# Kernel tuning notes

Hardware: AMD Instinct MI355X
Metric: run time of the kernel (lower is better)

Reference implementation:

```python
import jax, jax.numpy as jnp
import numpy as np

N, K_, D_ = 16384, 32, 128

def setup_inputs() -> dict:
    key = jax.random.key(0)
    k1, k2, k3 = jax.random.split(key, 3)
    x = jax.random.normal(k1, (1, N, D_), dtype=jnp.float32)
    codes = jax.random.normal(k2, (K_, D_), dtype=jnp.float32)
    scale = jax.random.uniform(k3, (K_,), dtype=jnp.float32)
    return {"x": x, "codes": codes, "scale": scale}

def reference(x, codes, scale):
    # x: (1, N, D) -> residuals R: (N, K, D)
    R = x[0][:, None, :] - codes[None, :, :]
    # scaled L2 norm (NOT squared) over D, scaled per-codeword by `scale`
    l2 = jnp.linalg.norm(R, axis=-1)            # (N, K)
    W = jax.nn.softmax(l2 * scale, axis=-1)     # softmax over K
    # aggregated encoding: (K, D)
    E = jnp.einsum('nk,nkd->kd', W, R)
    return E
```

## Files before the change

kernel.cpp:

```cpp
#include <hip/hip_runtime.h>

constexpr int N    = 16384;
constexpr int K    = 32;
constexpr int D    = 128;
constexpr int SPAD = K + 2;

typedef float f4 __attribute__((ext_vector_type(4)));

template <int CTRL>
__device__ __forceinline__ float dpp_add(float v) {
    int j = __builtin_amdgcn_update_dpp(0, __float_as_int(v), CTRL, 0xF, 0xF, false);
    return v + __int_as_float(j);
}
__device__ __forceinline__ float sum16(float v) {
    v = dpp_add<0xB1>(v);
    v = dpp_add<0x4E>(v);
    v = dpp_add<0x141>(v);
    v = dpp_add<0x140>(v);
    return v;
}

__global__ __launch_bounds__(256) void enc_partial(
    const float* __restrict__ x,
    const float* __restrict__ codes,
    const float* __restrict__ scale,
    float* __restrict__ ws,
    int nchunk)
{
    __shared__ float sc_lds[8][SPAD];
    __shared__ float w_lds[8][SPAD];

    const int tid = threadIdx.x;
    const int kg  = tid >> 4;
    const int dg  = tid & 15;
    const int d4  = dg << 2;
    const int k0  = kg << 1;

    const float4 cA0 = *reinterpret_cast<const float4*>(&codes[k0 * D + d4]);
    const float4 cA1 = *reinterpret_cast<const float4*>(&codes[k0 * D + 64 + d4]);
    const float4 cB0 = *reinterpret_cast<const float4*>(&codes[(k0 + 1) * D + d4]);
    const float4 cB1 = *reinterpret_cast<const float4*>(&codes[(k0 + 1) * D + 64 + d4]);
    const float sA = scale[k0];
    const float sB = scale[k0 + 1];

    float4 tA0 = make_float4(0.f, 0.f, 0.f, 0.f);
    float4 tA1 = tA0, tB0 = tA0, tB1 = tA0;
    float swA = 0.f, swB = 0.f;

    const float* xb = x + (long)blockIdx.x * nchunk * 8 * D;

    for (int c = 0; c < nchunk; ++c) {
        float4 xr[8][2];
        const float* xc = xb + c * 8 * D;
        #pragma unroll
        for (int n = 0; n < 8; ++n) {
            xr[n][0] = *reinterpret_cast<const float4*>(xc + n * D + d4);
            xr[n][1] = *reinterpret_cast<const float4*>(xc + n * D + 64 + d4);
        }

        #pragma unroll
        for (int n = 0; n < 8; ++n) {
            const float4 xa = xr[n][0];
            const float4 xb4 = xr[n][1];
            float r;
            float pA0 = 0.f, pA1 = 0.f, pB0 = 0.f, pB1 = 0.f;
            r = xa.x - cA0.x;  pA0 = fmaf(r, r, pA0);
            r = xa.y - cA0.y;  pA1 = fmaf(r, r, pA1);
            r = xa.z - cA0.z;  pA0 = fmaf(r, r, pA0);
            r = xa.w - cA0.w;  pA1 = fmaf(r, r, pA1);
            r = xb4.x - cA1.x; pA0 = fmaf(r, r, pA0);
            r = xb4.y - cA1.y; pA1 = fmaf(r, r, pA1);
            r = xb4.z - cA1.z; pA0 = fmaf(r, r, pA0);
            r = xb4.w - cA1.w; pA1 = fmaf(r, r, pA1);
            r = xa.x - cB0.x;  pB0 = fmaf(r, r, pB0);
            r = xa.y - cB0.y;  pB1 = fmaf(r, r, pB1);
            r = xa.z - cB0.z;  pB0 = fmaf(r, r, pB0);
            r = xa.w - cB0.w;  pB1 = fmaf(r, r, pB1);
            r = xb4.x - cB1.x; pB0 = fmaf(r, r, pB0);
            r = xb4.y - cB1.y; pB1 = fmaf(r, r, pB1);
            r = xb4.z - cB1.z; pB0 = fmaf(r, r, pB0);
            r = xb4.w - cB1.w; pB1 = fmaf(r, r, pB1);
            float pA = sum16(pA0 + pA1);
            float pB = sum16(pB0 + pB1);
            if (dg == 0) {
                sc_lds[n][k0]     = sqrtf(pA) * sA;
                sc_lds[n][k0 + 1] = sqrtf(pB) * sB;
            }
        }
        __syncthreads();

        {
            const int row = tid >> 5;
            const int q   = tid & 31;
            float s = sc_lds[row][q];
            float m = s;
            m = fmaxf(m, __shfl_xor(m, 1));
            m = fmaxf(m, __shfl_xor(m, 2));
            m = fmaxf(m, __shfl_xor(m, 4));
            m = fmaxf(m, __shfl_xor(m, 8));
            m = fmaxf(m, __shfl_xor(m, 16));
            const float LOG2E = 1.44269504088896f;
            float e = exp2f((s - m) * LOG2E);
            float sum = e;
            sum += __shfl_xor(sum, 1);
            sum += __shfl_xor(sum, 2);
            sum += __shfl_xor(sum, 4);
            sum += __shfl_xor(sum, 8);
            sum += __shfl_xor(sum, 16);
            w_lds[row][q] = e * (1.0f / sum);
        }
        __syncthreads();

        #pragma unroll
        for (int n = 0; n < 8; ++n) {
            const float2 w = *reinterpret_cast<const float2*>(&w_lds[n][k0]);
            const float4 xa = xr[n][0];
            const float4 xb4 = xr[n][1];
            tA0.x = fmaf(w.x, xa.x, tA0.x);
            tA0.y = fmaf(w.x, xa.y, tA0.y);
            tA0.z = fmaf(w.x, xa.z, tA0.z);
            tA0.w = fmaf(w.x, xa.w, tA0.w);
            tA1.x = fmaf(w.x, xb4.x, tA1.x);
            tA1.y = fmaf(w.x, xb4.y, tA1.y);
            tA1.z = fmaf(w.x, xb4.z, tA1.z);
            tA1.w = fmaf(w.x, xb4.w, tA1.w);
            tB0.x = fmaf(w.y, xa.x, tB0.x);
            tB0.y = fmaf(w.y, xa.y, tB0.y);
            tB0.z = fmaf(w.y, xa.z, tB0.z);
            tB0.w = fmaf(w.y, xa.w, tB0.w);
            tB1.x = fmaf(w.y, xb4.x, tB1.x);
            tB1.y = fmaf(w.y, xb4.y, tB1.y);
            tB1.z = fmaf(w.y, xb4.z, tB1.z);
            tB1.w = fmaf(w.y, xb4.w, tB1.w);
            swA += w.x;
            swB += w.y;
        }
        __syncthreads();
    }

    f4* o = reinterpret_cast<f4*>(ws + (long)blockIdx.x * (K * D) + k0 * D + d4);
    f4 e0 = { tA0.x - swA * cA0.x, tA0.y - swA * cA0.y,
              tA0.z - swA * cA0.z, tA0.w - swA * cA0.w };
    f4 e1 = { tA1.x - swA * cA1.x, tA1.y - swA * cA1.y,
              tA1.z - swA * cA1.z, tA1.w - swA * cA1.w };
    f4 e2 = { tB0.x - swB * cB0.x, tB0.y - swB * cB0.y,
              tB0.z - swB * cB0.z, tB0.w - swB * cB0.w };
    f4 e3 = { tB1.x - swB * cB1.x, tB1.y - swB * cB1.y,
              tB1.z - swB * cB1.z, tB1.w - swB * cB1.w };
    __builtin_nontemporal_store(e0, o);
    __builtin_nontemporal_store(e1, o + 16);
    __builtin_nontemporal_store(e2, o + 32);
    __builtin_nontemporal_store(e3, o + 48);
}

__global__ __launch_bounds__(256) void reduce2(
    const float* __restrict__ ws, float* __restrict__ out, int nrows)
{
    __shared__ f4 part[64][4];

    const int tid   = threadIdx.x;
    const int col   = tid & 3;
    const int slice = tid >> 2;
    const int gcol  = blockIdx.x * 4 + col;
    const int rpt   = nrows >> 6;

    const f4* P = reinterpret_cast<const f4*>(ws);
    f4 acc = { 0.f, 0.f, 0.f, 0.f };
    long base = (long)slice * rpt * 1024 + gcol;
    for (int r = 0; r < rpt; ++r) {
        f4 v = __builtin_nontemporal_load(P + base + (long)r * 1024);
        acc += v;
    }
    part[slice][col] = acc;
    __syncthreads();

    #pragma unroll
    for (int stride = 32; stride >= 1; stride >>= 1) {
        if (tid < stride * 4) {
            part[slice][col] += part[slice + stride][col];
        }
        __syncthreads();
    }
    if (tid < 4) {
        reinterpret_cast<f4*>(out)[blockIdx.x * 4 + tid] = part[0][tid];
    }
}

extern "C" void kernel_launch(void* const* d_in, const int* in_sizes, int n_in,
                              void* d_out, int out_size, void* d_ws, size_t ws_size,
                              hipStream_t stream) {
    const float* x     = (const float*)d_in[0];
    const float* codes = (const float*)d_in[1];
    const float* scale = (const float*)d_in[2];
    float* out = (float*)d_out;
    float* ws  = (float*)d_ws;

    int grid1 = 512;
    if (ws_size < (size_t)grid1 * K * D * sizeof(float)) grid1 = 128;
    const int nchunk = N / (grid1 * 8);

    enc_partial<<<grid1, 256, 0, stream>>>(x, codes, scale, ws, nchunk);
    reduce2<<<256, 256, 0, stream>>>(ws, out, grid1);
}
```

Measured before the change: 29.26 us.

## Expand squared distance via dot products, double-buffer LDS, use DPP reductions, enlarge grid

Computes the squared distance as |x|^2 - 2 x·c + |c|^2, with the codeword norms precomputed once into LDS, so the inner loop uses FMAs without residual subtractions. The sqrt and scale step moves into the softmax stage. The score and weight LDS buffers are double-buffered so the third barrier per chunk can be dropped, and the shuffle max and sum reductions are replaced with DPP-based ones. The grid grows to 1024 blocks when the workspace allows, with launch bounds set for occupancy. The expansion risks cancellation error, and the larger grid adds more partial rows for the reduce kernel to sum.

Result: faster. 28.11 us (-3.9%).

```diff
diff --git a/kernel.cpp b/kernel.cpp
--- a/kernel.cpp
+++ b/kernel.cpp
@@ -11,6 +11,11 @@
 __device__ __forceinline__ float dpp_add(float v) {
     int j = __builtin_amdgcn_update_dpp(0, __float_as_int(v), CTRL, 0xF, 0xF, false);
     return v + __int_as_float(j);
+}
+template <int CTRL>
+__device__ __forceinline__ float dpp_max(float v) {
+    int j = __builtin_amdgcn_update_dpp(0, __float_as_int(v), CTRL, 0xF, 0xF, false);
+    return fmaxf(v, __int_as_float(j));
 }
 __device__ __forceinline__ float sum16(float v) {
     v = dpp_add<0xB1>(v);
@@ -19,16 +24,24 @@
     v = dpp_add<0x140>(v);
     return v;
 }
-
-__global__ __launch_bounds__(256) void enc_partial(
+__device__ __forceinline__ float max16(float v) {
+    v = dpp_max<0xB1>(v);
+    v = dpp_max<0x4E>(v);
+    v = dpp_max<0x141>(v);
+    v = dpp_max<0x140>(v);
+    return v;
+}
+
+__global__ __launch_bounds__(256, 4) void enc_partial(
     const float* __restrict__ x,
     const float* __restrict__ codes,
     const float* __restrict__ scale,
     float* __restrict__ ws,
     int nchunk)
 {
-    __shared__ float sc_lds[8][SPAD];
-    __shared__ float w_lds[8][SPAD];
+    __shared__ float sc_lds[2][8][SPAD];
+    __shared__ float w_lds[2][8][SPAD];
+    __shared__ float cn2_lds[K];
 
     const int tid = threadIdx.x;
     const int kg  = tid >> 4;
@@ -40,8 +53,25 @@
     const float4 cA1 = *reinterpret_cast<const float4*>(&codes[k0 * D + 64 + d4]);
     const float4 cB0 = *reinterpret_cast<const float4*>(&codes[(k0 + 1) * D + d4]);
     const float4 cB1 = *reinterpret_cast<const float4*>(&codes[(k0 + 1) * D + 64 + d4]);
-    const float sA = scale[k0];
-    const float sB = scale[k0 + 1];
+
+    {
+        float pa = 0.f, pb = 0.f;
+        pa = fmaf(cA0.x, cA0.x, pa); pa = fmaf(cA0.y, cA0.y, pa);
+        pa = fmaf(cA0.z, cA0.z, pa); pa = fmaf(cA0.w, cA0.w, pa);
+        pa = fmaf(cA1.x, cA1.x, pa); pa = fmaf(cA1.y, cA1.y, pa);
+        pa = fmaf(cA1.z, cA1.z, pa); pa = fmaf(cA1.w, cA1.w, pa);
+        pb = fmaf(cB0.x, cB0.x, pb); pb = fmaf(cB0.y, cB0.y, pb);
+        pb = fmaf(cB0.z, cB0.z, pb); pb = fmaf(cB0.w, cB0.w, pb);
+        pb = fmaf(cB1.x, cB1.x, pb); pb = fmaf(cB1.y, cB1.y, pb);
+        pb = fmaf(cB1.z, cB1.z, pb); pb = fmaf(cB1.w, cB1.w, pb);
+        float cn2A = sum16(pa);
+        float cn2B = sum16(pb);
+        if (dg == 0) {
+            cn2_lds[k0]     = cn2A;
+            cn2_lds[k0 + 1] = cn2B;
+        }
+    }
+    const float sclq = scale[tid & 31];
 
     float4 tA0 = make_float4(0.f, 0.f, 0.f, 0.f);
     float4 tA1 = tA0, tB0 = tA0, tB1 = tA0;
@@ -50,6 +80,7 @@
     const float* xb = x + (long)blockIdx.x * nchunk * 8 * D;
 
     for (int c = 0; c < nchunk; ++c) {
+        const int p = c & 1;
         float4 xr[8][2];
         const float* xc = xb + c * 8 * D;
         #pragma unroll
@@ -62,29 +93,26 @@
         for (int n = 0; n < 8; ++n) {
             const float4 xa = xr[n][0];
             const float4 xb4 = xr[n][1];
-            float r;
-            float pA0 = 0.f, pA1 = 0.f, pB0 = 0.f, pB1 = 0.f;
-            r = xa.x - cA0.x;  pA0 = fmaf(r, r, pA0);
-            r = xa.y - cA0.y;  pA1 = fmaf(r, r, pA1);
-            r = xa.z - cA0.z;  pA0 = fmaf(r, r, pA0);
-            r = xa.w - cA0.w;  pA1 = fmaf(r, r, pA1);
-            r = xb4.x - cA1.x; pA0 = fmaf(r, r, pA0);
-            r = xb4.y - cA1.y; pA1 = fmaf(r, r, pA1);
-            r = xb4.z - cA1.z; pA0 = fmaf(r, r, pA0);
-            r = xb4.w - cA1.w; pA1 = fmaf(r, r, pA1);
-            r = xa.x - cB0.x;  pB0 = fmaf(r, r, pB0);
-            r = xa.y - cB0.y;  pB1 = fmaf(r, r, pB1);
-            r = xa.z - cB0.z;  pB0 = fmaf(r, r, pB0);
-            r = xa.w - cB0.w;  pB1 = fmaf(r, r, pB1);
-            r = xb4.x - cB1.x; pB0 = fmaf(r, r, pB0);
-            r = xb4.y - cB1.y; pB1 = fmaf(r, r, pB1);
-            r = xb4.z - cB1.z; pB0 = fmaf(r, r, pB0);
-            r = xb4.w - cB1.w; pB1 = fmaf(r, r, pB1);
-            float pA = sum16(pA0 + pA1);
-            float pB = sum16(pB0 + pB1);
+            float nx = 0.f, dA = 0.f, dB = 0.f;
+            nx = fmaf(xa.x, xa.x, nx);   nx = fmaf(xa.y, xa.y, nx);
+            nx = fmaf(xa.z, xa.z, nx);   nx = fmaf(xa.w, xa.w, nx);
+            nx = fmaf(xb4.x, xb4.x, nx); nx = fmaf(xb4.y, xb4.y, nx);
+            nx = fmaf(xb4.z, xb4.z, nx); nx = fmaf(xb4.w, xb4.w, nx);
+            dA = fmaf(xa.x, cA0.x, dA);  dA = fmaf(xa.y, cA0.y, dA);
+            dA = fmaf(xa.z, cA0.z, dA);  dA = fmaf(xa.w, cA0.w, dA);
+            dA = fmaf(xb4.x, cA1.x, dA); dA = fmaf(xb4.y, cA1.y, dA);
+            dA = fmaf(xb4.z, cA1.z, dA); dA = fmaf(xb4.w, cA1.w, dA);
+            dB = fmaf(xa.x, cB0.x, dB);  dB = fmaf(xa.y, cB0.y, dB);
+            dB = fmaf(xa.z, cB0.z, dB);  dB = fmaf(xa.w, cB0.w, dB);
+            dB = fmaf(xb4.x, cB1.x, dB); dB = fmaf(xb4.y, cB1.y, dB);
+            dB = fmaf(xb4.z, cB1.z, dB); dB = fmaf(xb4.w, cB1.w, dB);
+            float qA = fmaf(-2.f, dA, nx);
+            float qB = fmaf(-2.f, dB, nx);
+            qA = sum16(qA);
+            qB = sum16(qB);
             if (dg == 0) {
-                sc_lds[n][k0]     = sqrtf(pA) * sA;
-                sc_lds[n][k0 + 1] = sqrtf(pB) * sB;
+                sc_lds[p][n][k0]     = qA;
+                sc_lds[p][n][k0 + 1] = qB;
             }
         }
         __syncthreads();
@@ -92,28 +120,20 @@
         {
             const int row = tid >> 5;
             const int q   = tid & 31;
-            float s = sc_lds[row][q];
-            float m = s;
-            m = fmaxf(m, __shfl_xor(m, 1));
-            m = fmaxf(m, __shfl_xor(m, 2));
-            m = fmaxf(m, __shfl_xor(m, 4));
-            m = fmaxf(m, __shfl_xor(m, 8));
+            float sq = sc_lds[p][row][q];
+            float s  = sqrtf(fmaxf(sq + cn2_lds[q], 0.f)) * sclq;
+            float m = max16(s);
             m = fmaxf(m, __shfl_xor(m, 16));
-            const float LOG2E = 1.44269504088896f;
-            float e = exp2f((s - m) * LOG2E);
-            float sum = e;
-            sum += __shfl_xor(sum, 1);
-            sum += __shfl_xor(sum, 2);
-            sum += __shfl_xor(sum, 4);
-            sum += __shfl_xor(sum, 8);
+            float e = exp2f((s - m) * 1.44269504088896f);
+            float sum = sum16(e);
             sum += __shfl_xor(sum, 16);
-            w_lds[row][q] = e * (1.0f / sum);
+            w_lds[p][row][q] = e * (1.0f / sum);
         }
         __syncthreads();
 
         #pragma unroll
         for (int n = 0; n < 8; ++n) {
-            const float2 w = *reinterpret_cast<const float2*>(&w_lds[n][k0]);
+            const float2 w = *reinterpret_cast<const float2*>(&w_lds[p][n][k0]);
             const float4 xa = xr[n][0];
             const float4 xb4 = xr[n][1];
             tA0.x = fmaf(w.x, xa.x, tA0.x);
@@ -135,7 +155,6 @@
             swA += w.x;
             swB += w.y;
         }
-        __syncthreads();
     }
 
     f4* o = reinterpret_cast<f4*>(ws + (long)blockIdx.x * (K * D) + k0 * D + d4);
@@ -195,7 +214,8 @@
     float* out = (float*)d_out;
     float* ws  = (float*)d_ws;
 
-    int grid1 = 512;
+    int grid1 = 1024;
+    if (ws_size < (size_t)grid1 * K * D * sizeof(float)) grid1 = 512;
     if (ws_size < (size_t)grid1 * K * D * sizeof(float)) grid1 = 128;
     const int nchunk = N / (grid1 * 8);
 
```
